# Kernel optimization log

Hardware: AMD Instinct MI355X
Metric: run time of the kernel (lower is better)

## Reference

```python
import jax, jax.numpy as jnp
import numpy as np

B, H, W, S = 4, 512, 512, 40
DZ = 0.1            # slice thickness
FOCUS_SLICE = 25    # back-propagation slice count
Z_PLANE = 2.0       # focus plane offset
PAD = 32            # output crop


def setup_inputs() -> dict:
    key = jax.random.key(0)
    ks = jax.random.split(key, 8)
    sample_re = jax.random.normal(ks[0], (B, H, W, S), jnp.float32) * 0.01
    sample_im = jax.random.normal(ks[1], (B, H, W, S), jnp.float32) * 0.01
    planewave_re = jax.random.normal(ks[2], (B, H, W), jnp.float32)
    planewave_im = jax.random.normal(ks[3], (B, H, W), jnp.float32)
    # kz strictly positive so 1/(2*kz) is finite (mask + nan-fix kept for faithfulness)
    kz = jax.random.uniform(ks[4], (H, W), jnp.float32) + 0.5
    otf_abs = jax.random.uniform(ks[5], (H, W), jnp.float32)
    green_mask = (jax.random.uniform(ks[6], (H, W), jnp.float32) < 0.7).astype(jnp.float32)
    otf_phase = jax.random.normal(ks[7], (H, W), jnp.float32) * 0.1
    return dict(sample_re=sample_re, sample_im=sample_im,
                planewave_re=planewave_re, planewave_im=planewave_im,
                kz=kz, otf_abs=otf_abs, green_mask=green_mask, otf_phase=otf_phase)


def reference(sample_re, sample_im, planewave_re, planewave_im, kz, otf_abs, green_mask, otf_phase):
    sample = (sample_re + 1j * sample_im).astype(jnp.complex64)        # [B,H,W,S]
    planewave = (planewave_re + 1j * planewave_im).astype(jnp.complex64)  # [B,H,W]
    kzc = kz.astype(jnp.complex64)

    # module constants: prop_kernel = exp(prop_kernel_pha * dz), prop_kernel_pha = 1j*kz
    prop_kernel = jnp.exp(1j * kzc * DZ)                               # [H,W]
    green = (1j * prop_kernel / (2.0 * kzc)) * green_mask.astype(jnp.complex64)
    green = jnp.where(jnp.isnan(green), jnp.zeros((), green.dtype), green)

    # _propegate_to_last_slice_Multi_Born (oblique_factor=None)
    inc0 = jnp.fft.fft2(planewave)                                     # fft over last two dims
    sample_s = jnp.moveaxis(sample, -1, 0)                             # [S,B,H,W]

    def step(inc, slab):
        u = inc * prop_kernel
        scat = green * jnp.fft.fft2(jnp.fft.ifft2(inc) * slab * DZ)
        return u + scat, None

    inc, _ = jax.lax.scan(step, inc0, sample_s)

    # _propegate_to_center_focus_slice
    pk_center = jnp.conj(prop_kernel ** FOCUS_SLICE)
    pk_focus = prop_kernel ** (Z_PLANE / DZ)
    inc = inc * pk_center * pk_focus

    # _pupil_constrain_abs_square_output with OTF_input provided
    otf_update = (otf_abs * jnp.exp(1j * otf_phase)).astype(jnp.complex64)
    out = jnp.fft.ifft2(inc * otf_update[None])
    return jnp.abs(out)[:, PAD:-PAD, PAD:-PAD]                          # [B, H-2*PAD, W-2*PAD]
```

## Files before the change

### kernel.cpp

```cpp
#include <hip/hip_runtime.h>
#include <math.h>

#define HW_ (512 * 512)

__device__ inline float2 cadd(float2 a, float2 b){ return make_float2(a.x+b.x, a.y+b.y); }
__device__ inline float2 csub(float2 a, float2 b){ return make_float2(a.x-b.x, a.y-b.y); }
__device__ inline float2 cmulf(float2 a, float2 b){ return make_float2(a.x*b.x-a.y*b.y, a.x*b.y+a.y*b.x); }
__device__ inline float bf2f(unsigned short u){ return __uint_as_float(((unsigned int)u) << 16); }
__device__ inline unsigned short f2bf(float f){
    unsigned int x = __float_as_uint(f);
    x += 0x7fffu + ((x >> 16) & 1u);
    return (unsigned short)(x >> 16);
}

template<bool INV>
__device__ inline void dft8(const float2 a[8], float2 X[8]) {
    const float C = 0.70710678118654752440f;
    float2 t0 = cadd(a[0], a[4]), t4 = csub(a[0], a[4]);
    float2 t1 = cadd(a[1], a[5]), d1 = csub(a[1], a[5]);
    float2 t2 = cadd(a[2], a[6]), d2 = csub(a[2], a[6]);
    float2 t3 = cadd(a[3], a[7]), d3 = csub(a[3], a[7]);
    float2 t5, t6, t7;
    if (!INV) {
        t5 = make_float2(C*(d1.x + d1.y), C*(d1.y - d1.x));
        t6 = make_float2(d2.y, -d2.x);
        t7 = make_float2(C*(d3.y - d3.x), -C*(d3.x + d3.y));
    } else {
        t5 = make_float2(C*(d1.x - d1.y), C*(d1.y + d1.x));
        t6 = make_float2(-d2.y, d2.x);
        t7 = make_float2(-C*(d3.x + d3.y), C*(d3.x - d3.y));
    }
    float2 u0 = cadd(t0, t2), u2 = csub(t0, t2);
    float2 u1 = cadd(t1, t3), e3 = csub(t1, t3);
    float2 u3 = INV ? make_float2(-e3.y, e3.x) : make_float2(e3.y, -e3.x);
    float2 u4 = cadd(t4, t6), u6 = csub(t4, t6);
    float2 u5 = cadd(t5, t7), e7 = csub(t5, t7);
    float2 u7 = INV ? make_float2(-e7.y, e7.x) : make_float2(e7.y, -e7.x);
    X[0] = cadd(u0, u1); X[4] = csub(u0, u1);
    X[2] = cadd(u2, u3); X[6] = csub(u2, u3);
    X[1] = cadd(u4, u5); X[5] = csub(u4, u5);
    X[3] = cadd(u6, u7); X[7] = csub(u6, u7);
}

template<bool INV>
__device__ inline void fft512_reg(float2 a[8], float2* __restrict__ xch,
                                  int lane, float2 T1, float2 T2)
{
    float2 tw1 = INV ? make_float2(T1.x, -T1.y) : T1;
    float2 tw2 = INV ? make_float2(T2.x, -T2.y) : T2;
    const int rdo = lane + (lane >> 3);
    float2 b[8];

    dft8<INV>(a, b);
    { float2 w = tw1;
      #pragma unroll
      for (int k = 1; k < 8; ++k) { b[k] = cmulf(b[k], w); w = cmulf(w, tw1); } }
    #pragma unroll
    for (int k = 0; k < 8; ++k) xch[9*lane + k] = b[k];
    __asm__ volatile("s_waitcnt lgkmcnt(0)" ::: "memory");
    #pragma unroll
    for (int j = 0; j < 8; ++j) a[j] = xch[rdo + 72*j];

    dft8<INV>(a, b);
    { float2 w = tw2;
      #pragma unroll
      for (int k = 1; k < 8; ++k) { b[k] = cmulf(b[k], w); w = cmulf(w, tw2); } }
    { const int wbase = (lane & 7) + 72 * (lane >> 3);
      #pragma unroll
      for (int k = 0; k < 8; ++k) xch[wbase + 9*k] = b[k]; }
    __asm__ volatile("s_waitcnt lgkmcnt(0)" ::: "memory");
    #pragma unroll
    for (int j = 0; j < 8; ++j) b[j] = xch[rdo + 72*j];

    dft8<INV>(b, a);
}

__global__ __launch_bounds__(256)
void k_pre(const float* __restrict__ kz, const float* __restrict__ otfa,
           const float* __restrict__ gmask, const float* __restrict__ otfp,
           float2* __restrict__ propT, float2* __restrict__ greenT,
           float2* __restrict__ MT)
{
    __shared__ float2 tp[32*33], tg[32*33], tm[32*33];
    const int tid = threadIdx.x;
    const int w0 = (blockIdx.x & 15) << 5;
    const int h0 = (blockIdx.x >> 4) << 5;
    const int ww = tid & 31, hh = tid >> 5;
    #pragma unroll
    for (int p = 0; p < 4; ++p) {
        int h = hh + p*8;
        int idx = (h0 + h)*512 + w0 + ww;
        float k = kz[idx];
        float sn, cs; __sincosf(k * 0.1f, &sn, &cs);
        float inv2 = 0.5f / k * gmask[idx];
        float phase = otfp[idx] - k * 0.5f;
        float s2, c2; __sincosf(phase, &s2, &c2);
        float oa = otfa[idx];
        tp[h*33 + ww] = make_float2(cs, sn);
        tg[h*33 + ww] = make_float2(-sn*inv2, cs*inv2);
        tm[h*33 + ww] = make_float2(oa*c2, oa*s2);
    }
    __syncthreads();
    #pragma unroll
    for (int p = 0; p < 4; ++p) {
        int wrow = hh + p*8;
        size_t o = (size_t)(w0 + wrow)*512 + h0 + ww;
        propT[o]  = tp[ww*33 + wrow];
        greenT[o] = tg[ww*33 + wrow];
        MT[o]     = tm[ww*33 + wrow];
    }
}

__global__ __launch_bounds__(256)
void k_transpose(const float* __restrict__ sre, const float* __restrict__ sim,
                 ushort2* __restrict__ sampT)
{
    __shared__ ushort2 tile[40 * 129];
    const int bh = blockIdx.x;
    const int b = bh >> 9, h = bh & 511;
    const size_t src_base = (size_t)bh * (512 * 40);
    const float2* sre2 = (const float2*)(sre + src_base);
    const float2* sim2 = (const float2*)(sim + src_base);
    for (int chunk = 0; chunk < 4; ++chunk) {
        const int w0 = chunk * 128;
        const int base2 = w0 * 20;
        __syncthreads();
        for (int j = threadIdx.x; j < 128 * 20; j += 256) {
            float2 re = sre2[base2 + j];
            float2 im = sim2[base2 + j];
            int w = j / 20;
            int s = (j - w * 20) * 2;
            tile[s*129 + w]       = make_ushort2(f2bf(re.x), f2bf(im.x));
            tile[(s+1)*129 + w]   = make_ushort2(f2bf(re.y), f2bf(im.y));
        }
        __syncthreads();
        for (int j = threadIdx.x; j < 40 * 64; j += 256) {
            int s = j >> 6, w2 = (j & 63) << 1;
            ushort2 u0 = tile[s*129 + w2], u1 = tile[s*129 + w2 + 1];
            *(ushort4*)&sampT[(((size_t)s*4 + b)*512 + h)*512 + w0 + w2] =
                make_ushort4(u0.x, u0.y, u1.x, u1.y);
        }
    }
}

__global__ __launch_bounds__(256)
void k_row(float2* __restrict__ fld,
           const float* __restrict__ pwre, const float* __restrict__ pwim,
           const ushort2* __restrict__ sampT,
           float* __restrict__ finout,
           int mode, int slice)
{
    __shared__ float2 xchall[4 * 576];
    const int tid = threadIdx.x, lane = tid & 63, wv = tid >> 6;
    float2* xch = &xchall[wv * 576];
    float s1, c1, s2, c2;
    __sincosf(-6.2831853071795864769f * (float)lane / 512.0f, &s1, &c1);
    __sincosf(-6.2831853071795864769f * (float)(lane >> 3) / 64.0f, &s2, &c2);
    const float2 T1 = make_float2(c1, s1), T2 = make_float2(c2, s2);

    const int r = blockIdx.x * 4 + wv;
    int b, h;
    if (mode == 2) { b = r / 448; h = 32 + (r - b * 448); }
    else           { b = r >> 9;  h = r & 511; }
    const size_t rbase = ((size_t)b * 512 + h) * 512;
    float2 a[8];

    if (mode == 0) {
        #pragma unroll
        for (int j = 0; j < 8; ++j) {
            int w = lane + (j << 6);
            a[j] = make_float2(pwre[rbase + w], pwim[rbase + w]);
        }
        fft512_reg<false>(a, xch, lane, T1, T2);
        #pragma unroll
        for (int j = 0; j < 8; ++j) fld[rbase + lane + (j << 6)] = a[j];
        return;
    }

    #pragma unroll
    for (int j = 0; j < 8; ++j) a[j] = fld[rbase + lane + (j << 6)];
    fft512_reg<true>(a, xch, lane, T1, T2);

    if (mode == 2) {
        float* orow = finout + ((size_t)b * 448 + (h - 32)) * 448;
        #pragma unroll
        for (int j = 0; j < 8; ++j) {
            int w = lane + (j << 6);
            if (w >= 32 && w < 480) {
                float2 v = a[j];
                orow[w - 32] = sqrtf(v.x*v.x + v.y*v.y) * (1.0f / 512.0f);
            }
        }
        return;
    }

    const float scale = 0.1f / 512.0f;
    const size_t sbase = (((size_t)slice * 4 + b) * 512 + h) * 512;
    #pragma unroll
    for (int j = 0; j < 8; ++j) {
        int w = lane + (j << 6);
        ushort2 u = sampT[sbase + w];
        float sr = bf2f(u.x), si = bf2f(u.y);
        float2 v = a[j];
        a[j] = make_float2((v.x*sr - v.y*si) * scale, (v.x*si + v.y*sr) * scale);
    }
    fft512_reg<false>(a, xch, lane, T1, T2);
    #pragma unroll
    for (int j = 0; j < 8; ++j) fld[rbase + lane + (j << 6)] = a[j];
}

__global__ __launch_bounds__(512)
void k_col(float2* __restrict__ fld,
           float2* __restrict__ incT,
           const float2* __restrict__ propT, const float2* __restrict__ greenT,
           const float2* __restrict__ MT, int mode)
{
    __shared__ float2 tile[512 * 9];
    const int tid = threadIdx.x;
    const int lane = tid & 63, wv = tid >> 6;
    const int b = blockIdx.x >> 6;
    const int w0 = (blockIdx.x & 63) << 3;
    const int c = tid & 7, hb = tid >> 3;
    const size_t gbase = (size_t)b * HW_ + w0;

    float s1, c1, s2, c2;
    __sincosf(-6.2831853071795864769f * (float)lane / 512.0f, &s1, &c1);
    __sincosf(-6.2831853071795864769f * (float)(lane >> 3) / 64.0f, &s2, &c2);
    const float2 T1 = make_float2(c1, s1), T2 = make_float2(c2, s2);

    #pragma unroll
    for (int j = 0; j < 8; ++j) {
        int h = hb + (j << 6);
        tile[h*9 + c] = fld[gbase + (size_t)h * 512 + c];
    }
    __syncthreads();
    float2 a[8];
    const int w = w0 + wv;
    #pragma unroll
    for (int j = 0; j < 8; ++j) a[j] = tile[(lane + (j << 6)) * 9 + wv];
    __syncthreads();
    float2* xch = &tile[wv * 576];

    fft512_reg<false>(a, xch, lane, T1, T2);

    const size_t ibase = ((size_t)b * 512 + w) * 512;
    const size_t pbase = (size_t)w * 512;
    if (mode == 0) {
        #pragma unroll
        for (int k = 0; k < 8; ++k) incT[ibase + lane + (k << 6)] = a[k];
        return;
    }
    #pragma unroll
    for (int k = 0; k < 8; ++k) {
        int h = lane + (k << 6);
        float2 p  = propT[pbase + h];
        float2 g  = greenT[pbase + h];
        float2 io = incT[ibase + h];
        float2 nw = make_float2(p.x*io.x - p.y*io.y + g.x*a[k].x - g.y*a[k].y,
                                p.x*io.y + p.y*io.x + g.x*a[k].y + g.y*a[k].x);
        if (mode == 2) nw = cmulf(nw, MT[pbase + h]);
        else           incT[ibase + h] = nw;
        a[k] = nw;
    }

    fft512_reg<true>(a, xch, lane, T1, T2);
    __syncthreads();
    const float inv = 1.0f / 512.0f;
    #pragma unroll
    for (int k = 0; k < 8; ++k)
        tile[(lane + (k << 6)) * 9 + wv] = make_float2(a[k].x * inv, a[k].y * inv);
    __syncthreads();
    #pragma unroll
    for (int j = 0; j < 8; ++j) {
        int h = hb + (j << 6);
        fld[gbase + (size_t)h * 512 + c] = tile[h*9 + c];
    }
}

extern "C" void kernel_launch(void* const* d_in, const int* in_sizes, int n_in,
                              void* d_out, int out_size, void* d_ws, size_t ws_size,
                              hipStream_t stream)
{
    (void)in_sizes; (void)n_in; (void)out_size; (void)ws_size;
    const float* sre   = (const float*)d_in[0];
    const float* simg  = (const float*)d_in[1];
    const float* pwre  = (const float*)d_in[2];
    const float* pwim  = (const float*)d_in[3];
    const float* kz    = (const float*)d_in[4];
    const float* otfa  = (const float*)d_in[5];
    const float* gmask = (const float*)d_in[6];
    const float* otfp  = (const float*)d_in[7];

    char* ws = (char*)d_ws;
    size_t off = 0;
    float2* propT  = (float2*)(ws + off); off += (size_t)HW_ * 8;
    float2* greenT = (float2*)(ws + off); off += (size_t)HW_ * 8;
    float2* MT     = (float2*)(ws + off); off += (size_t)HW_ * 8;
    float2* incT   = (float2*)(ws + off); off += (size_t)4 * HW_ * 8;
    float2* fld    = (float2*)(ws + off); off += (size_t)4 * HW_ * 8;
    ushort2* sampT = (ushort2*)(ws + off);

    k_pre<<<256, 256, 0, stream>>>(kz, otfa, gmask, otfp, propT, greenT, MT);
    k_transpose<<<2048, 256, 0, stream>>>(sre, simg, sampT);

    k_row<<<512, 256, 0, stream>>>(fld, pwre, pwim, nullptr, nullptr, 0, 0);
    k_col<<<256, 512, 0, stream>>>(fld, incT, propT, greenT, MT, 0);

    for (int s = 0; s < 40; ++s) {
        k_row<<<512, 256, 0, stream>>>(fld, nullptr, nullptr, sampT, nullptr, 1, s);
        k_col<<<256, 512, 0, stream>>>(fld, incT, propT, greenT, MT, (s == 39) ? 2 : 1);
    }
    k_row<<<448, 256, 0, stream>>>(fld, nullptr, nullptr, nullptr, (float*)d_out, 2, 0);
}
```

Measured before the change: 1.355 ms.

## Fuse per-slice row/column FFT kernels into one persistent cooperative kernel

Replaces the 80+ separate row and column FFT launches with a single cooperative kernel of 256 blocks that loops over all 40 slices, using grid-wide syncs between the row and column phases. The incident field, propagation and Green kernels stay in registers across slices instead of being reloaded from global memory, and the intermediate field is stored as packed fp16 to halve traffic. The transpose kernel is also rewritten to use scalar loads. This trades launch overhead and memory traffic for grid-sync costs, reduced precision (fp16 range and accuracy on FFT intermediates), and occupancy limited to 256 blocks.

```diff
diff --git a/kernel.cpp b/kernel.cpp
--- a/kernel.cpp
+++ b/kernel.cpp
@@ -1,5 +1,9 @@
 #include <hip/hip_runtime.h>
+#include <hip/hip_fp16.h>
+#include <hip/hip_cooperative_groups.h>
 #include <math.h>
+
+namespace cg = cooperative_groups;
 
 #define HW_ (512 * 512)
 
@@ -11,6 +15,14 @@
     unsigned int x = __float_as_uint(f);
     x += 0x7fffu + ((x >> 16) & 1u);
     return (unsigned short)(x >> 16);
+}
+__device__ inline unsigned int pack_h2(float2 v){
+    __half2 h = __floats2half2_rn(v.x, v.y);
+    return *(unsigned int*)&h;
+}
+__device__ inline float2 unpack_h2(unsigned int u){
+    __half2 h = *(__half2*)&u;
+    return make_float2(__low2float(h), __high2float(h));
 }
 
 template<bool INV>
@@ -119,70 +131,147 @@
     const int bh = blockIdx.x;
     const int b = bh >> 9, h = bh & 511;
     const size_t src_base = (size_t)bh * (512 * 40);
-    const float2* sre2 = (const float2*)(sre + src_base);
-    const float2* sim2 = (const float2*)(sim + src_base);
     for (int chunk = 0; chunk < 4; ++chunk) {
         const int w0 = chunk * 128;
-        const int base2 = w0 * 20;
-        __syncthreads();
-        for (int j = threadIdx.x; j < 128 * 20; j += 256) {
-            float2 re = sre2[base2 + j];
-            float2 im = sim2[base2 + j];
-            int w = j / 20;
-            int s = (j - w * 20) * 2;
-            tile[s*129 + w]       = make_ushort2(f2bf(re.x), f2bf(im.x));
-            tile[(s+1)*129 + w]   = make_ushort2(f2bf(re.y), f2bf(im.y));
-        }
-        __syncthreads();
-        for (int j = threadIdx.x; j < 40 * 64; j += 256) {
-            int s = j >> 6, w2 = (j & 63) << 1;
-            ushort2 u0 = tile[s*129 + w2], u1 = tile[s*129 + w2 + 1];
-            *(ushort4*)&sampT[(((size_t)s*4 + b)*512 + h)*512 + w0 + w2] =
-                make_ushort4(u0.x, u0.y, u1.x, u1.y);
-        }
-    }
-}
-
-__global__ __launch_bounds__(256)
-void k_row(float2* __restrict__ fld,
-           const float* __restrict__ pwre, const float* __restrict__ pwim,
-           const ushort2* __restrict__ sampT,
-           float* __restrict__ finout,
-           int mode, int slice)
-{
-    __shared__ float2 xchall[4 * 576];
+        __syncthreads();
+        for (int j = threadIdx.x; j < 128 * 40; j += 256) {
+            float re = sre[src_base + (size_t)w0 * 40 + j];
+            float im = sim[src_base + (size_t)w0 * 40 + j];
+            int w = j / 40;
+            int s = j - w * 40;
+            tile[s * 129 + w] = make_ushort2(f2bf(re), f2bf(im));
+        }
+        __syncthreads();
+        for (int j = threadIdx.x; j < 128 * 40; j += 256) {
+            int s = j >> 7, w = j & 127;
+            sampT[(((size_t)s * 4 + b) * 512 + h) * 512 + w0 + w] = tile[s * 129 + w];
+        }
+    }
+}
+
+__global__ __launch_bounds__(512)
+void k_main(unsigned int* __restrict__ fldH,
+            const float2* __restrict__ propT, const float2* __restrict__ greenT,
+            const float2* __restrict__ MT,
+            const ushort2* __restrict__ sampT,
+            const float* __restrict__ pwre, const float* __restrict__ pwim,
+            float* __restrict__ out)
+{
+    __shared__ float2 lds[8 * 576];
+    unsigned int* tileu = (unsigned int*)lds;
+    cg::grid_group grid = cg::this_grid();
+
     const int tid = threadIdx.x, lane = tid & 63, wv = tid >> 6;
-    float2* xch = &xchall[wv * 576];
+    const int bk = blockIdx.x;
+    float2* xch = &lds[wv * 576];
+
     float s1, c1, s2, c2;
     __sincosf(-6.2831853071795864769f * (float)lane / 512.0f, &s1, &c1);
     __sincosf(-6.2831853071795864769f * (float)(lane >> 3) / 64.0f, &s2, &c2);
     const float2 T1 = make_float2(c1, s1), T2 = make_float2(c2, s2);
 
-    const int r = blockIdx.x * 4 + wv;
-    int b, h;
-    if (mode == 2) { b = r / 448; h = 32 + (r - b * 448); }
-    else           { b = r >> 9;  h = r & 511; }
-    const size_t rbase = ((size_t)b * 512 + h) * 512;
-    float2 a[8];
-
-    if (mode == 0) {
+    const int r = bk * 8 + wv;
+    const int rb = r >> 9, rh = r & 511;
+    const size_t rbase = (size_t)r * 512;
+    const int cb = bk >> 6;
+    const int cw0 = (bk & 63) << 3;
+    const size_t cbase = (size_t)cb * HW_ + cw0;
+    const size_t pbase = (size_t)(cw0 + wv) * 512;
+    const int cc = tid & 7, hb = tid >> 3;
+
+    float2 p[8], g[8], inc[8], a[8];
+    #pragma unroll
+    for (int k = 0; k < 8; ++k) {
+        p[k] = propT[pbase + lane + (k << 6)];
+        g[k] = greenT[pbase + lane + (k << 6)];
+    }
+
+    #pragma unroll
+    for (int j = 0; j < 8; ++j) {
+        int w = lane + (j << 6);
+        a[j] = make_float2(pwre[rbase + w], pwim[rbase + w]);
+    }
+    fft512_reg<false>(a, xch, lane, T1, T2);
+    #pragma unroll
+    for (int j = 0; j < 8; ++j) fldH[rbase + lane + (j << 6)] = pack_h2(a[j]);
+    grid.sync();
+
+    #pragma unroll
+    for (int j = 0; j < 8; ++j) {
+        int h = hb + (j << 6);
+        tileu[h*9 + cc] = fldH[cbase + (size_t)h * 512 + cc];
+    }
+    __syncthreads();
+    #pragma unroll
+    for (int j = 0; j < 8; ++j) a[j] = unpack_h2(tileu[(lane + (j << 6))*9 + wv]);
+    __syncthreads();
+    fft512_reg<false>(a, xch, lane, T1, T2);
+    #pragma unroll
+    for (int k = 0; k < 8; ++k) inc[k] = a[k];
+    grid.sync();
+
+    for (int s = 0; s < 40; ++s) {
+        const size_t sbase = (size_t)s * 4 * HW_ + rbase;
+        unsigned int su[8];
+        #pragma unroll
+        for (int j = 0; j < 8; ++j)
+            su[j] = *(const unsigned int*)&sampT[sbase + lane + (j << 6)];
+        #pragma unroll
+        for (int j = 0; j < 8; ++j) a[j] = unpack_h2(fldH[rbase + lane + (j << 6)]);
+        fft512_reg<true>(a, xch, lane, T1, T2);
+        const float scale = 0.1f / 512.0f;
         #pragma unroll
         for (int j = 0; j < 8; ++j) {
-            int w = lane + (j << 6);
-            a[j] = make_float2(pwre[rbase + w], pwim[rbase + w]);
+            float sr = bf2f((unsigned short)(su[j] & 0xffffu));
+            float si = bf2f((unsigned short)(su[j] >> 16));
+            float2 v = a[j];
+            a[j] = make_float2((v.x*sr - v.y*si) * scale, (v.x*si + v.y*sr) * scale);
         }
         fft512_reg<false>(a, xch, lane, T1, T2);
         #pragma unroll
-        for (int j = 0; j < 8; ++j) fld[rbase + lane + (j << 6)] = a[j];
-        return;
-    }
-
-    #pragma unroll
-    for (int j = 0; j < 8; ++j) a[j] = fld[rbase + lane + (j << 6)];
+        for (int j = 0; j < 8; ++j) fldH[rbase + lane + (j << 6)] = pack_h2(a[j]);
+        grid.sync();
+
+        #pragma unroll
+        for (int j = 0; j < 8; ++j) {
+            int h = hb + (j << 6);
+            tileu[h*9 + cc] = fldH[cbase + (size_t)h * 512 + cc];
+        }
+        __syncthreads();
+        #pragma unroll
+        for (int j = 0; j < 8; ++j) a[j] = unpack_h2(tileu[(lane + (j << 6))*9 + wv]);
+        __syncthreads();
+        fft512_reg<false>(a, xch, lane, T1, T2);
+        #pragma unroll
+        for (int k = 0; k < 8; ++k) {
+            float2 s5 = a[k], io = inc[k];
+            float2 nw = make_float2(
+                p[k].x*io.x - p[k].y*io.y + g[k].x*s5.x - g[k].y*s5.y,
+                p[k].x*io.y + p[k].y*io.x + g[k].x*s5.y + g[k].y*s5.x);
+            if (s == 39) nw = cmulf(nw, MT[pbase + lane + (k << 6)]);
+            inc[k] = nw;
+            a[k] = nw;
+        }
+        fft512_reg<true>(a, xch, lane, T1, T2);
+        __syncthreads();
+        const float inv = 1.0f / 512.0f;
+        #pragma unroll
+        for (int k = 0; k < 8; ++k)
+            tileu[(lane + (k << 6))*9 + wv] = pack_h2(make_float2(a[k].x*inv, a[k].y*inv));
+        __syncthreads();
+        #pragma unroll
+        for (int j = 0; j < 8; ++j) {
+            int h = hb + (j << 6);
+            fldH[cbase + (size_t)h * 512 + cc] = tileu[h*9 + cc];
+        }
+        grid.sync();
+    }
+
+    #pragma unroll
+    for (int j = 0; j < 8; ++j) a[j] = unpack_h2(fldH[rbase + lane + (j << 6)]);
     fft512_reg<true>(a, xch, lane, T1, T2);
-
-    if (mode == 2) {
-        float* orow = finout + ((size_t)b * 448 + (h - 32)) * 448;
+    if (rh >= 32 && rh < 480) {
+        float* orow = out + ((size_t)rb * 448 + (rh - 32)) * 448;
         #pragma unroll
         for (int j = 0; j < 8; ++j) {
             int w = lane + (j << 6);
@@ -191,89 +280,6 @@
                 orow[w - 32] = sqrtf(v.x*v.x + v.y*v.y) * (1.0f / 512.0f);
             }
         }
-        return;
-    }
-
-    const float scale = 0.1f / 512.0f;
-    const size_t sbase = (((size_t)slice * 4 + b) * 512 + h) * 512;
-    #pragma unroll
-    for (int j = 0; j < 8; ++j) {
-        int w = lane + (j << 6);
-        ushort2 u = sampT[sbase + w];
-        float sr = bf2f(u.x), si = bf2f(u.y);
-        float2 v = a[j];
-        a[j] = make_float2((v.x*sr - v.y*si) * scale, (v.x*si + v.y*sr) * scale);
-    }
-    fft512_reg<false>(a, xch, lane, T1, T2);
-    #pragma unroll
-    for (int j = 0; j < 8; ++j) fld[rbase + lane + (j << 6)] = a[j];
-}
-
-__global__ __launch_bounds__(512)
-void k_col(float2* __restrict__ fld,
-           float2* __restrict__ incT,
-           const float2* __restrict__ propT, const float2* __restrict__ greenT,
-           const float2* __restrict__ MT, int mode)
-{
-    __shared__ float2 tile[512 * 9];
-    const int tid = threadIdx.x;
-    const int lane = tid & 63, wv = tid >> 6;
-    const int b = blockIdx.x >> 6;
-    const int w0 = (blockIdx.x & 63) << 3;
-    const int c = tid & 7, hb = tid >> 3;
-    const size_t gbase = (size_t)b * HW_ + w0;
-
-    float s1, c1, s2, c2;
-    __sincosf(-6.2831853071795864769f * (float)lane / 512.0f, &s1, &c1);
-    __sincosf(-6.2831853071795864769f * (float)(lane >> 3) / 64.0f, &s2, &c2);
-    const float2 T1 = make_float2(c1, s1), T2 = make_float2(c2, s2);
-
-    #pragma unroll
-    for (int j = 0; j < 8; ++j) {
-        int h = hb + (j << 6);
-        tile[h*9 + c] = fld[gbase + (size_t)h * 512 + c];
-    }
-    __syncthreads();
-    float2 a[8];
-    const int w = w0 + wv;
-    #pragma unroll
-    for (int j = 0; j < 8; ++j) a[j] = tile[(lane + (j << 6)) * 9 + wv];
-    __syncthreads();
-    float2* xch = &tile[wv * 576];
-
-    fft512_reg<false>(a, xch, lane, T1, T2);
-
-    const size_t ibase = ((size_t)b * 512 + w) * 512;
-    const size_t pbase = (size_t)w * 512;
-    if (mode == 0) {
-        #pragma unroll
-        for (int k = 0; k < 8; ++k) incT[ibase + lane + (k << 6)] = a[k];
-        return;
-    }
-    #pragma unroll
-    for (int k = 0; k < 8; ++k) {
-        int h = lane + (k << 6);
-        float2 p  = propT[pbase + h];
-        float2 g  = greenT[pbase + h];
-        float2 io = incT[ibase + h];
-        float2 nw = make_float2(p.x*io.x - p.y*io.y + g.x*a[k].x - g.y*a[k].y,
-                                p.x*io.y + p.y*io.x + g.x*a[k].y + g.y*a[k].x);
-        if (mode == 2) nw = cmulf(nw, MT[pbase + h]);
-        else           incT[ibase + h] = nw;
-        a[k] = nw;
-    }
-
-    fft512_reg<true>(a, xch, lane, T1, T2);
-    __syncthreads();
-    const float inv = 1.0f / 512.0f;
-    #pragma unroll
-    for (int k = 0; k < 8; ++k)
-        tile[(lane + (k << 6)) * 9 + wv] = make_float2(a[k].x * inv, a[k].y * inv);
-    __syncthreads();
-    #pragma unroll
-    for (int j = 0; j < 8; ++j) {
-        int h = hb + (j << 6);
-        fld[gbase + (size_t)h * 512 + c] = tile[h*9 + c];
     }
 }
 
@@ -296,19 +302,15 @@
     float2* propT  = (float2*)(ws + off); off += (size_t)HW_ * 8;
     float2* greenT = (float2*)(ws + off); off += (size_t)HW_ * 8;
     float2* MT     = (float2*)(ws + off); off += (size_t)HW_ * 8;
-    float2* incT   = (float2*)(ws + off); off += (size_t)4 * HW_ * 8;
-    float2* fld    = (float2*)(ws + off); off += (size_t)4 * HW_ * 8;
+    unsigned int* fldH = (unsigned int*)(ws + off); off += (size_t)4 * HW_ * 4;
     ushort2* sampT = (ushort2*)(ws + off);
 
     k_pre<<<256, 256, 0, stream>>>(kz, otfa, gmask, otfp, propT, greenT, MT);
     k_transpose<<<2048, 256, 0, stream>>>(sre, simg, sampT);
 
-    k_row<<<512, 256, 0, stream>>>(fld, pwre, pwim, nullptr, nullptr, 0, 0);
-    k_col<<<256, 512, 0, stream>>>(fld, incT, propT, greenT, MT, 0);
-
-    for (int s = 0; s < 40; ++s) {
-        k_row<<<512, 256, 0, stream>>>(fld, nullptr, nullptr, sampT, nullptr, 1, s);
-        k_col<<<256, 512, 0, stream>>>(fld, incT, propT, greenT, MT, (s == 39) ? 2 : 1);
-    }
-    k_row<<<448, 256, 0, stream>>>(fld, nullptr, nullptr, nullptr, (float*)d_out, 2, 0);
-}
+    float* outp = (float*)d_out;
+    void* args[] = { (void*)&fldH, (void*)&propT, (void*)&greenT, (void*)&MT,
+                     (void*)&sampT, (void*)&pwre, (void*)&pwim, (void*)&outp };
+    hipLaunchCooperativeKernel((const void*)k_main, dim3(256), dim3(512),
+                               args, 0, stream);
+}
```

New measurement: 3.659 ms. +170.1%, slower.
